# Kernel optimization log

Measured on AMD Instinct MI355X. Metric: run time of the kernel, lower is better.

Reference implementation:

```python
import jax, jax.numpy as jnp
import numpy as np

S, B, D, H, WIN, L = 8192, 4, 512, 8, 64, 6
HD = D // H
EPS = 1e-5


def setup_inputs() -> dict:
    key = jax.random.key(0)
    ks = jax.random.split(key, 6)
    s = 0.02
    return {
        "src": jax.random.normal(ks[0], (S, B, D), jnp.float32),
        "Wqkv": jax.random.normal(ks[1], (L, 3 * D, D), jnp.float32) * s,
        "bqkv": jnp.zeros((L, 3 * D), jnp.float32),
        "Wo": jax.random.normal(ks[2], (L, D, D), jnp.float32) * s,
        "bo": jnp.zeros((L, D), jnp.float32),
        "W1": jax.random.normal(ks[3], (L, 4 * D, D), jnp.float32) * s,
        "bf1": jnp.zeros((L, 4 * D), jnp.float32),
        "W2": jax.random.normal(ks[4], (L, D, 4 * D), jnp.float32) * s,
        "bf2": jnp.zeros((L, D), jnp.float32),
        "g1": jnp.ones((L, D), jnp.float32),
        "beta1": jnp.zeros((L, D), jnp.float32),
        "g2": jnp.ones((L, D), jnp.float32),
        "beta2": jnp.zeros((L, D), jnp.float32),
    }


def layernorm(x, g, b):
    m = jnp.mean(x, axis=-1, keepdims=True)
    v = jnp.mean(jnp.square(x - m), axis=-1, keepdims=True)
    return (x - m) * jax.lax.rsqrt(v + EPS) * g + b


def _forward(src, Wqkv, bqkv, Wo, bo, W1, bf1, W2, bf2, g1, beta1, g2, beta2):
    NW = S // WIN
    scale = 1.0 / np.sqrt(HD)
    x = src
    for l in range(L):
        qkv = x @ Wqkv[l].T + bqkv[l]                      # (S,B,3D)
        q, k, v = jnp.split(qkv, 3, axis=-1)
        win = lambda t: t.reshape(NW, WIN, B, H, HD)       # (NW,W,B,H,hd)
        q = win(q) * scale
        k = win(k)
        v = win(v)
        att = jax.nn.softmax(jnp.einsum('nqbhd,nkbhd->nbhqk', q, k), axis=-1)
        o = jnp.einsum('nbhqk,nkbhd->nqbhd', att, v).reshape(S, B, D)
        o = o @ Wo[l].T + bo[l]
        x = layernorm(x + o, g1[l], beta1[l])
        # FFN with ReLU (hidden = 4*d_model)
        f = jax.nn.relu(x @ W1[l].T + bf1[l]) @ W2[l].T + bf2[l]
        x = layernorm(x + f, g2[l], beta2[l])
    return x


def reference(src, Wqkv, bqkv, Wo, bo, W1, bf1, W2, bf2, g1, beta1, g2, beta2):
    return _forward(src, Wqkv, bqkv, Wo, bo, W1, bf1, W2, bf2, g1, beta1, g2, beta2)
```

## Files before the change

### kernel.cpp

```cpp
#include <hip/hip_runtime.h>
#include <hip/hip_bf16.h>

typedef __bf16 bf16x8 __attribute__((ext_vector_type(8)));
typedef float f32x4 __attribute__((ext_vector_type(4)));

static constexpr int NT = 32768;
static constexpr int D_ = 512;
static constexpr int D3 = 1536;
static constexpr int DF = 2048;
static constexpr int L_ = 6;

#define AS1 __attribute__((address_space(1)))
#define AS3 __attribute__((address_space(3)))

__device__ __forceinline__ void gload_lds16(const void* g, void* l) {
  __builtin_amdgcn_global_load_lds((const AS1 void*)g, (AS3 void*)l, 16, 0, 0);
}

template<int K, int NTILES, bool RELU>
__global__ __launch_bounds__(256, 2) void gemm_bt(
    const __hip_bfloat16* __restrict__ A,
    const __hip_bfloat16* __restrict__ W,
    const float* __restrict__ bias,
    __hip_bfloat16* __restrict__ Cout) {
  __shared__ __align__(16) __hip_bfloat16 lds[2 * 128 * 64];
  __hip_bfloat16* ldsA = lds;
  __hip_bfloat16* ldsB = lds + 128 * 64;
  const int t = threadIdx.x;
  const int l = t & 63, w = t >> 6;
  const int lrow = l & 15, lhi = l >> 4;

  const int lin = blockIdx.x;
  const int wg = (lin & 7) * ((int)gridDim.x >> 3) + (lin >> 3);
  const int tm0 = (wg / NTILES) * 128, tn0 = (wg % NTILES) * 128;
  const int wr = (w >> 1) * 64, wc = (w & 1) * 64;

  f32x4 acc[4][4] = {};

  const int nkt = K / 64;
  for (int kt = 0; kt < nkt; ++kt) {
    const int kbase = kt * 64;
    if (kt) __syncthreads();
#pragma unroll
    for (int i = 0; i < 4; ++i) {
      int slot = i * 256 + t;
      int row = slot >> 3, unit = slot & 7;
      int gc = kbase + ((unit ^ (row & 7)) << 3);
      gload_lds16(A + (size_t)(tm0 + row) * K + gc,
                  (char*)ldsA + i * 4096 + w * 1024);
    }
#pragma unroll
    for (int i = 0; i < 4; ++i) {
      int slot = i * 256 + t;
      int row = slot >> 3, unit = slot & 7;
      int gc = kbase + ((unit ^ (row & 7)) << 3);
      gload_lds16(W + (size_t)(tn0 + row) * K + gc,
                  (char*)ldsB + i * 4096 + w * 1024);
    }
    __syncthreads();

    bf16x8 af[4][2], bfr[4][2];
#pragma unroll
    for (int mi = 0; mi < 4; ++mi) {
      int r = wr + mi * 16 + lrow;
#pragma unroll
      for (int ks = 0; ks < 2; ++ks) {
        int unit = ks * 4 + lhi;
        af[mi][ks] = *(const bf16x8*)((const char*)ldsA + r * 128 + ((unit ^ (r & 7)) << 4));
      }
    }
#pragma unroll
    for (int ni = 0; ni < 4; ++ni) {
      int r = wc + ni * 16 + lrow;
#pragma unroll
      for (int ks = 0; ks < 2; ++ks) {
        int unit = ks * 4 + lhi;
        bfr[ni][ks] = *(const bf16x8*)((const char*)ldsB + r * 128 + ((unit ^ (r & 7)) << 4));
      }
    }
#pragma unroll
    for (int mi = 0; mi < 4; ++mi)
#pragma unroll
      for (int ni = 0; ni < 4; ++ni) {
        acc[mi][ni] = __builtin_amdgcn_mfma_f32_16x16x32_bf16(af[mi][0], bfr[ni][0], acc[mi][ni], 0, 0, 0);
        acc[mi][ni] = __builtin_amdgcn_mfma_f32_16x16x32_bf16(af[mi][1], bfr[ni][1], acc[mi][ni], 0, 0, 0);
      }
  }

  __syncthreads();
  char* ep = (char*)lds + w * 8192;
#pragma unroll
  for (int ni = 0; ni < 4; ++ni) {
    float bv = bias[tn0 + wc + ni * 16 + lrow];
#pragma unroll
    for (int mi = 0; mi < 4; ++mi) {
#pragma unroll
      for (int j = 0; j < 4; ++j) {
        float v = acc[mi][ni][j] + bv;
        if (RELU) v = fmaxf(v, 0.f);
        *(__hip_bfloat16*)(ep + (mi * 16 + lhi * 4 + j) * 128 + (ni * 16 + lrow) * 2) =
            __float2bfloat16(v);
      }
    }
  }
  const int er = l >> 3, ec = l & 7;
#pragma unroll
  for (int p = 0; p < 8; ++p) {
    int r = p * 8 + er;
    uint4 vv = *(const uint4*)(ep + r * 128 + ec * 16);
    *(uint4*)&Cout[(size_t)(tm0 + wr + r) * (NTILES * 128) + tn0 + wc + ec * 8] = vv;
  }
}

__global__ __launch_bounds__(128) void attn_win(
    const __hip_bfloat16* __restrict__ qkv, __hip_bfloat16* __restrict__ o) {
  __shared__ __align__(16) char lds[2 * 18432];
  const int t = threadIdx.x, l = t & 63, w = t >> 6;
  char* vt = lds + w * 18432;
  char* pl = vt + 9216;
  const int wid = blockIdx.x * 2 + w;
  const int h = wid & 7, b = (wid >> 3) & 3, nw = wid >> 5;
  const int lrow = l & 15, lhi = l >> 4;
  const __hip_bfloat16* qp = qkv + (size_t)(nw * 256 + b) * 1536 + h * 64;
  const __hip_bfloat16* kp = qp + 512;
  const __hip_bfloat16* vp = qp + 1024;

  {
    const int d0 = (l & 7) * 8;
    const int r0 = l >> 3;
#pragma unroll
    for (int i = 0; i < 8; ++i) {
      int r = r0 + i * 8;
      union { uint4 u; __hip_bfloat16 e[8]; } vv;
      vv.u = *(const uint4*)(vp + (size_t)r * 6144 + d0);
#pragma unroll
      for (int j = 0; j < 8; ++j)
        *(__hip_bfloat16*)(vt + ((d0 + j) * 72 + r) * 2) = vv.e[j];
    }
  }

  bf16x8 qf[4][2], kf[4][2];
#pragma unroll
  for (int mi = 0; mi < 4; ++mi)
#pragma unroll
    for (int ks = 0; ks < 2; ++ks) {
      int r = mi * 16 + lrow;
      int d = ks * 32 + lhi * 8;
      qf[mi][ks] = __builtin_bit_cast(bf16x8, *(const uint4*)(qp + (size_t)r * 6144 + d));
      kf[mi][ks] = __builtin_bit_cast(bf16x8, *(const uint4*)(kp + (size_t)r * 6144 + d));
    }

  f32x4 s[4][4] = {};
#pragma unroll
  for (int mi = 0; mi < 4; ++mi)
#pragma unroll
    for (int ni = 0; ni < 4; ++ni) {
      s[mi][ni] = __builtin_amdgcn_mfma_f32_16x16x32_bf16(qf[mi][0], kf[ni][0], s[mi][ni], 0, 0, 0);
      s[mi][ni] = __builtin_amdgcn_mfma_f32_16x16x32_bf16(qf[mi][1], kf[ni][1], s[mi][ni], 0, 0, 0);
    }

#pragma unroll
  for (int mi = 0; mi < 4; ++mi)
#pragma unroll
    for (int j = 0; j < 4; ++j) {
      float mx = s[mi][0][j];
#pragma unroll
      for (int ni = 1; ni < 4; ++ni) mx = fmaxf(mx, s[mi][ni][j]);
      mx = fmaxf(mx, __shfl_xor(mx, 1));
      mx = fmaxf(mx, __shfl_xor(mx, 2));
      mx = fmaxf(mx, __shfl_xor(mx, 4));
      mx = fmaxf(mx, __shfl_xor(mx, 8));
      float p[4], sum = 0.f;
#pragma unroll
      for (int ni = 0; ni < 4; ++ni) { p[ni] = __expf(s[mi][ni][j] - mx); sum += p[ni]; }
      sum += __shfl_xor(sum, 1);
      sum += __shfl_xor(sum, 2);
      sum += __shfl_xor(sum, 4);
      sum += __shfl_xor(sum, 8);
      float inv = 1.f / sum;
      int row = mi * 16 + lhi * 4 + j;
#pragma unroll
      for (int ni = 0; ni < 4; ++ni)
        *(__hip_bfloat16*)(pl + (row * 72 + ni * 16 + lrow) * 2) =
            __float2bfloat16(p[ni] * inv);
    }

  bf16x8 pf[4][2], vf[4][2];
#pragma unroll
  for (int mi = 0; mi < 4; ++mi)
#pragma unroll
    for (int ks = 0; ks < 2; ++ks)
      pf[mi][ks] = *(const bf16x8*)(pl + ((mi * 16 + lrow) * 72 + ks * 32 + lhi * 8) * 2);
#pragma unroll
  for (int ni = 0; ni < 4; ++ni)
#pragma unroll
    for (int ks = 0; ks < 2; ++ks)
      vf[ni][ks] = *(const bf16x8*)(vt + ((ni * 16 + lrow) * 72 + ks * 32 + lhi * 8) * 2);

  f32x4 acc[4][4] = {};
#pragma unroll
  for (int mi = 0; mi < 4; ++mi)
#pragma unroll
    for (int ni = 0; ni < 4; ++ni) {
      acc[mi][ni] = __builtin_amdgcn_mfma_f32_16x16x32_bf16(pf[mi][0], vf[ni][0], acc[mi][ni], 0, 0, 0);
      acc[mi][ni] = __builtin_amdgcn_mfma_f32_16x16x32_bf16(pf[mi][1], vf[ni][1], acc[mi][ni], 0, 0, 0);
    }

  __hip_bfloat16* op = o + (size_t)(nw * 256 + b) * 512 + h * 64;
#pragma unroll
  for (int mi = 0; mi < 4; ++mi)
#pragma unroll
    for (int ni = 0; ni < 4; ++ni) {
      int col = ni * 16 + lrow;
#pragma unroll
      for (int j = 0; j < 4; ++j) {
        int row = mi * 16 + lhi * 4 + j;
        op[(size_t)row * 2048 + col] = __float2bfloat16(acc[mi][ni][j]);
      }
    }
}

__global__ __launch_bounds__(256) void ln_res(
    float* __restrict__ x, const __hip_bfloat16* __restrict__ f,
    const float* __restrict__ g, const float* __restrict__ be,
    __hip_bfloat16* __restrict__ xb) {
  const int w = threadIdx.x >> 6, l = threadIdx.x & 63;
  const size_t row = (size_t)blockIdx.x * 4 + w;
  float* xr = x + row * 512;
  const int c = l * 8;
  float4 a0 = *(const float4*)(xr + c);
  float4 a1 = *(const float4*)(xr + c + 4);
  union { uint4 u; __hip_bfloat16 e[8]; } fb;
  fb.u = *(const uint4*)(f + row * 512 + c);
  float v[8] = {a0.x + __bfloat162float(fb.e[0]), a0.y + __bfloat162float(fb.e[1]),
                a0.z + __bfloat162float(fb.e[2]), a0.w + __bfloat162float(fb.e[3]),
                a1.x + __bfloat162float(fb.e[4]), a1.y + __bfloat162float(fb.e[5]),
                a1.z + __bfloat162float(fb.e[6]), a1.w + __bfloat162float(fb.e[7])};
  float sum = 0.f, sq = 0.f;
#pragma unroll
  for (int j = 0; j < 8; ++j) { sum += v[j]; sq += v[j] * v[j]; }
#pragma unroll
  for (int m = 1; m < 64; m <<= 1) {
    sum += __shfl_xor(sum, m);
    sq += __shfl_xor(sq, m);
  }
  float mean = sum * (1.f / 512.f);
  float var = sq * (1.f / 512.f) - mean * mean;
  float rs = rsqrtf(var + 1e-5f);
  float4 g0 = *(const float4*)(g + c);
  float4 g1v = *(const float4*)(g + c + 4);
  float4 e0 = *(const float4*)(be + c);
  float4 e1 = *(const float4*)(be + c + 4);
  float gg[8] = {g0.x, g0.y, g0.z, g0.w, g1v.x, g1v.y, g1v.z, g1v.w};
  float ee[8] = {e0.x, e0.y, e0.z, e0.w, e1.x, e1.y, e1.z, e1.w};
  float y[8];
  __hip_bfloat16 hb[8];
#pragma unroll
  for (int j = 0; j < 8; ++j) {
    y[j] = (v[j] - mean) * rs * gg[j] + ee[j];
    hb[j] = __float2bfloat16(y[j]);
  }
  float4 o0 = {y[0], y[1], y[2], y[3]};
  float4 o1 = {y[4], y[5], y[6], y[7]};
  *(float4*)(xr + c) = o0;
  *(float4*)(xr + c + 4) = o1;
  *(uint4*)((char*)(xb + row * 512 + c)) = *(uint4*)hb;
}

__global__ void bfc(const float* __restrict__ xm, __hip_bfloat16* __restrict__ xb) {
  int i = blockIdx.x * 256 + threadIdx.x;
  float4 v = ((const float4*)xm)[i];
  __hip_bfloat16 hb[4] = {__float2bfloat16(v.x), __float2bfloat16(v.y),
                          __float2bfloat16(v.z), __float2bfloat16(v.w)};
  ((uint2*)xb)[i] = *(uint2*)hb;
}

__global__ void convq(const float* __restrict__ wq, __hip_bfloat16* __restrict__ o) {
  int i = blockIdx.x * 256 + threadIdx.x;
  float4 v = ((const float4*)wq)[i];
  int e = i * 4;
  float sc = (((e >> 9) % 1536) < 512) ? 0.125f : 1.f;
  __hip_bfloat16 hb[4] = {__float2bfloat16(v.x * sc), __float2bfloat16(v.y * sc),
                          __float2bfloat16(v.z * sc), __float2bfloat16(v.w * sc)};
  ((uint2*)o)[i] = *(uint2*)hb;
}

__global__ void convw(const float* __restrict__ s, __hip_bfloat16* __restrict__ o) {
  int i = blockIdx.x * 256 + threadIdx.x;
  float4 v = ((const float4*)s)[i];
  __hip_bfloat16 hb[4] = {__float2bfloat16(v.x), __float2bfloat16(v.y),
                          __float2bfloat16(v.z), __float2bfloat16(v.w)};
  ((uint2*)o)[i] = *(uint2*)hb;
}

__global__ void scaleb(const float* __restrict__ b, float* __restrict__ o) {
  int i = blockIdx.x * 256 + threadIdx.x;
  o[i] = b[i] * (((i % 1536) < 512) ? 0.125f : 1.f);
}

extern "C" void kernel_launch(void* const* d_in, const int* in_sizes, int n_in,
                              void* d_out, int out_size, void* d_ws, size_t ws_size,
                              hipStream_t stream) {
  const float* src  = (const float*)d_in[0];
  const float* Wqkv = (const float*)d_in[1];
  const float* bqkv = (const float*)d_in[2];
  const float* Wo   = (const float*)d_in[3];
  const float* bo   = (const float*)d_in[4];
  const float* W1   = (const float*)d_in[5];
  const float* bf1  = (const float*)d_in[6];
  const float* W2   = (const float*)d_in[7];
  const float* bf2  = (const float*)d_in[8];
  const float* g1   = (const float*)d_in[9];
  const float* be1  = (const float*)d_in[10];
  const float* g2   = (const float*)d_in[11];
  const float* be2  = (const float*)d_in[12];
  float* x = (float*)d_out;

  char* ws = (char*)d_ws;
  size_t off = 0;
  auto alloc = [&](size_t bytes) {
    char* p = ws + off;
    off += (bytes + 255) & ~(size_t)255;
    return p;
  };

  const size_t wq_b = (size_t)L_ * D3 * D_ * 2;
  const size_t wo_b = (size_t)L_ * D_ * D_ * 2;
  const size_t w1_b = (size_t)L_ * DF * D_ * 2;
  const size_t w2_b = (size_t)L_ * D_ * DF * 2;
  auto al = [](size_t v) { return (v + 255) & ~(size_t)255; };
  const size_t persist = al(wq_b) + al(wo_b) + al(w1_b) + al(w2_b) + al(L_ * D3 * 4);

  int CT = NT;
  while (CT > 2048 && persist + (size_t)CT * 6144 + 65536 > ws_size) CT >>= 1;

  __hip_bfloat16* wqkvb = (__hip_bfloat16*)alloc(wq_b);
  __hip_bfloat16* wob   = (__hip_bfloat16*)alloc(wo_b);
  __hip_bfloat16* w1b   = (__hip_bfloat16*)alloc(w1_b);
  __hip_bfloat16* w2b   = (__hip_bfloat16*)alloc(w2_b);
  float*          bqs   = (float*)alloc((size_t)L_ * D3 * 4);
  __hip_bfloat16* xbf   = (__hip_bfloat16*)alloc((size_t)CT * 512 * 2);
  __hip_bfloat16* R     = (__hip_bfloat16*)alloc((size_t)CT * 2048 * 2);
  __hip_bfloat16* OB    = (__hip_bfloat16*)alloc((size_t)CT * 512 * 2);

  hipMemcpyAsync(x, src, (size_t)NT * 512 * 4, hipMemcpyDeviceToDevice, stream);
  convq<<<L_ * D3 * D_ / 4 / 256, 256, 0, stream>>>(Wqkv, wqkvb);
  convw<<<L_ * D_ * D_ / 4 / 256, 256, 0, stream>>>(Wo, wob);
  convw<<<L_ * DF * D_ / 4 / 256, 256, 0, stream>>>(W1, w1b);
  convw<<<L_ * D_ * DF / 4 / 256, 256, 0, stream>>>(W2, w2b);
  scaleb<<<L_ * D3 / 256, 256, 0, stream>>>(bqkv, bqs);

  const int nch = NT / CT;
  for (int c = 0; c < nch; ++c) {
    float* xm = x + (size_t)c * CT * 512;
    bfc<<<CT / 2, 256, 0, stream>>>(xm, xbf);
    for (int l = 0; l < L_; ++l) {
      gemm_bt<512, 12, false><<<(CT / 128) * 12, 256, 0, stream>>>(
          xbf, wqkvb + (size_t)l * D3 * D_, bqs + l * D3, R);
      attn_win<<<CT / 16, 128, 0, stream>>>(R, OB);
      gemm_bt<512, 4, false><<<(CT / 128) * 4, 256, 0, stream>>>(
          OB, wob + (size_t)l * D_ * D_, bo + l * D_, R);
      ln_res<<<CT / 4, 256, 0, stream>>>(xm, R, g1 + l * D_, be1 + l * D_, xbf);
      gemm_bt<512, 16, true><<<(CT / 128) * 16, 256, 0, stream>>>(
          xbf, w1b + (size_t)l * DF * D_, bf1 + l * DF, R);
      gemm_bt<2048, 4, false><<<(CT / 128) * 4, 256, 0, stream>>>(
          R, w2b + (size_t)l * D_ * DF, bf2 + l * D_, OB);
      ln_res<<<CT / 4, 256, 0, stream>>>(xm, OB, g2 + l * D_, be2 + l * D_, xbf);
    }
  }
}
```

Measured before the change: 2.143 ms.

## Replace 128x128 GEMM with double-buffered 256x256 tile, 8-wave pipelined kernel

Replaces the single-buffered 128x128 GEMM with a 256x256-tile, 512-thread kernel that double-buffers K tiles in 128KB of LDS. Global-to-LDS loads for later tiles are interleaved with the MFMA phases using explicit waitcnt, barriers and setprio. The larger tile raises data reuse per load, and the overlap hides load latency behind compute. The output epilogue also gains an XOR swizzle to avoid LDS bank conflicts. The cost is heavy LDS use, which limits occupancy to about one block per CU, and fewer blocks in the grid for the narrow GEMMs.

Result: faster. 2.024 ms (-5.6%).

```diff
diff --git a/kernel.cpp b/kernel.cpp
--- a/kernel.cpp
+++ b/kernel.cpp
@@ -17,98 +17,137 @@
   __builtin_amdgcn_global_load_lds((const AS1 void*)g, (AS3 void*)l, 16, 0, 0);
 }
 
-template<int K, int NTILES, bool RELU>
-__global__ __launch_bounds__(256, 2) void gemm_bt(
+template<int K, int NTN, bool RELU>
+__global__ __launch_bounds__(512, 2) void gemm256(
     const __hip_bfloat16* __restrict__ A,
     const __hip_bfloat16* __restrict__ W,
     const float* __restrict__ bias,
     __hip_bfloat16* __restrict__ Cout) {
-  __shared__ __align__(16) __hip_bfloat16 lds[2 * 128 * 64];
-  __hip_bfloat16* ldsA = lds;
-  __hip_bfloat16* ldsB = lds + 128 * 64;
+  __shared__ __align__(16) char lds[131072];
   const int t = threadIdx.x;
   const int l = t & 63, w = t >> 6;
   const int lrow = l & 15, lhi = l >> 4;
+  const int wr = w >> 2, wc = w & 3;
 
   const int lin = blockIdx.x;
   const int wg = (lin & 7) * ((int)gridDim.x >> 3) + (lin >> 3);
-  const int tm0 = (wg / NTILES) * 128, tn0 = (wg % NTILES) * 128;
-  const int wr = (w >> 1) * 64, wc = (w & 1) * 64;
-
-  f32x4 acc[4][4] = {};
-
-  const int nkt = K / 64;
-  for (int kt = 0; kt < nkt; ++kt) {
-    const int kbase = kt * 64;
-    if (kt) __syncthreads();
-#pragma unroll
-    for (int i = 0; i < 4; ++i) {
-      int slot = i * 256 + t;
-      int row = slot >> 3, unit = slot & 7;
-      int gc = kbase + ((unit ^ (row & 7)) << 3);
-      gload_lds16(A + (size_t)(tm0 + row) * K + gc,
-                  (char*)ldsA + i * 4096 + w * 1024);
-    }
-#pragma unroll
-    for (int i = 0; i < 4; ++i) {
-      int slot = i * 256 + t;
-      int row = slot >> 3, unit = slot & 7;
-      int gc = kbase + ((unit ^ (row & 7)) << 3);
-      gload_lds16(W + (size_t)(tn0 + row) * K + gc,
-                  (char*)ldsB + i * 4096 + w * 1024);
-    }
-    __syncthreads();
-
-    bf16x8 af[4][2], bfr[4][2];
-#pragma unroll
-    for (int mi = 0; mi < 4; ++mi) {
-      int r = wr + mi * 16 + lrow;
-#pragma unroll
-      for (int ks = 0; ks < 2; ++ks) {
-        int unit = ks * 4 + lhi;
-        af[mi][ks] = *(const bf16x8*)((const char*)ldsA + r * 128 + ((unit ^ (r & 7)) << 4));
+  const int tm0 = (wg / NTN) * 256, tn0 = (wg % NTN) * 256;
+
+  constexpr int NKT = K / 64;
+  constexpr int NIT = NKT / 2;
+  constexpr int N = NTN * 256;
+
+  const int srow = t >> 3;
+  const int sun = t & 7;
+
+  auto stage = [&](int buf, int reg, const __hip_bfloat16* P, int grow0, int tile) {
+    const int kb = tile * 64;
+    char* dst = lds + (buf * 4 + reg) * 16384 + w * 1024;
+#pragma unroll
+    for (int pass = 0; pass < 2; ++pass) {
+      int rl = pass * 64 + srow;
+      int u = sun ^ (rl & 7);
+      gload_lds16(P + (size_t)(grow0 + rl) * K + kb + u * 8, dst + pass * 8192);
+    }
+  };
+  auto rdA = [&](int buf, int m, int ks) -> bf16x8 {
+    int r = m * 16 + lrow;
+    return *(const bf16x8*)(lds + (buf * 4 + wr) * 16384 + r * 128 +
+                            (((ks * 4 + lhi) ^ (r & 7)) << 4));
+  };
+  auto rdB = [&](int buf, int n, int ks) -> bf16x8 {
+    int r = (wc & 1) * 64 + n * 16 + lrow;
+    return *(const bf16x8*)(lds + (buf * 4 + 2 + (wc >> 1)) * 16384 + r * 128 +
+                            (((ks * 4 + lhi) ^ (r & 7)) << 4));
+  };
+
+  f32x4 acc[8][4] = {};
+  bf16x8 bfrag[4][2], afrag[2][2];
+
+  stage(0, 2, W, tn0, 0);
+  stage(0, 3, W, tn0 + 128, 0);
+  stage(0, 0, A, tm0, 0);
+  stage(0, 1, A, tm0 + 128, 0);
+  stage(1, 2, W, tn0, 1);
+  stage(1, 3, W, tn0 + 128, 1);
+  asm volatile("s_waitcnt vmcnt(4)" ::: "memory");
+  __builtin_amdgcn_s_barrier();
+
+#define GPHASE(BUF, MB, RB, STG, VMS)                                       \
+  {                                                                          \
+    if (RB) {                                                                \
+      _Pragma("unroll") for (int n = 0; n < 4; ++n)                          \
+          _Pragma("unroll") for (int ks = 0; ks < 2; ++ks)                   \
+              bfrag[n][ks] = rdB(BUF, n, ks);                                \
+    }                                                                        \
+    _Pragma("unroll") for (int ks = 0; ks < 2; ++ks) {                       \
+      afrag[0][ks] = rdA(BUF, MB, ks);                                       \
+      afrag[1][ks] = rdA(BUF, MB + 1, ks);                                   \
+    }                                                                        \
+    STG;                                                                     \
+    VMS;                                                                     \
+    __builtin_amdgcn_sched_barrier(0);                                       \
+    __builtin_amdgcn_s_barrier();                                            \
+    asm volatile("s_waitcnt lgkmcnt(0)" ::: "memory");                       \
+    __builtin_amdgcn_sched_barrier(0);                                       \
+    __builtin_amdgcn_s_setprio(1);                                           \
+    _Pragma("unroll") for (int n = 0; n < 4; ++n)                            \
+        _Pragma("unroll") for (int ks = 0; ks < 2; ++ks) {                   \
+      acc[MB][n] = __builtin_amdgcn_mfma_f32_16x16x32_bf16(                  \
+          afrag[0][ks], bfrag[n][ks], acc[MB][n], 0, 0, 0);                  \
+      acc[MB + 1][n] = __builtin_amdgcn_mfma_f32_16x16x32_bf16(              \
+          afrag[1][ks], bfrag[n][ks], acc[MB + 1][n], 0, 0, 0);              \
+    }                                                                        \
+    __builtin_amdgcn_s_setprio(0);                                           \
+    __builtin_amdgcn_sched_barrier(0);                                       \
+    __builtin_amdgcn_s_barrier();                                            \
+  }
+
+#define VM_CNT                                              \
+  if (more) {                                               \
+    asm volatile("s_waitcnt vmcnt(4)" ::: "memory");        \
+  } else {                                                  \
+    asm volatile("s_waitcnt vmcnt(0)" ::: "memory");        \
+  }
+
+  for (int it = 0; it < NIT; ++it) {
+    const int t0 = 2 * it, t1 = 2 * it + 1;
+    const bool more = (it + 1 < NIT);
+    GPHASE(0, 0, 1, { stage(1, 0, A, tm0, t1); stage(1, 1, A, tm0 + 128, t1); }, );
+    GPHASE(0, 2, 0, { if (more) stage(0, 2, W, tn0, t0 + 2); }, );
+    GPHASE(0, 4, 0, { if (more) stage(0, 3, W, tn0 + 128, t0 + 2); }, );
+    GPHASE(0, 6, 0, , VM_CNT);
+    GPHASE(1, 0, 1, { if (more) stage(0, 0, A, tm0, t0 + 2); }, );
+    GPHASE(1, 2, 0, { if (more) stage(0, 1, A, tm0 + 128, t0 + 2); }, );
+    GPHASE(1, 4, 0, { if (more) stage(1, 2, W, tn0, t1 + 2); }, );
+    GPHASE(1, 6, 0, { if (more) stage(1, 3, W, tn0 + 128, t1 + 2); }, VM_CNT);
+  }
+#undef GPHASE
+#undef VM_CNT
+
+  char* ep = lds + w * 16384;
+#pragma unroll
+  for (int n = 0; n < 4; ++n) {
+    float bv = bias[tn0 + wc * 64 + n * 16 + lrow];
+#pragma unroll
+    for (int m = 0; m < 8; ++m)
+#pragma unroll
+      for (int j = 0; j < 4; ++j) {
+        float v = acc[m][n][j] + bv;
+        if (RELU) v = fmaxf(v, 0.f);
+        int row = m * 16 + lhi * 4 + j;
+        int col = n * 16 + lrow;
+        *(__hip_bfloat16*)(ep + row * 128 + (((col >> 3) ^ (row & 7)) << 4) +
+                           (col & 7) * 2) = __float2bfloat16(v);
       }
-    }
-#pragma unroll
-    for (int ni = 0; ni < 4; ++ni) {
-      int r = wc + ni * 16 + lrow;
-#pragma unroll
-      for (int ks = 0; ks < 2; ++ks) {
-        int unit = ks * 4 + lhi;
-        bfr[ni][ks] = *(const bf16x8*)((const char*)ldsB + r * 128 + ((unit ^ (r & 7)) << 4));
-      }
-    }
-#pragma unroll
-    for (int mi = 0; mi < 4; ++mi)
-#pragma unroll
-      for (int ni = 0; ni < 4; ++ni) {
-        acc[mi][ni] = __builtin_amdgcn_mfma_f32_16x16x32_bf16(af[mi][0], bfr[ni][0], acc[mi][ni], 0, 0, 0);
-        acc[mi][ni] = __builtin_amdgcn_mfma_f32_16x16x32_bf16(af[mi][1], bfr[ni][1], acc[mi][ni], 0, 0, 0);
-      }
-  }
-
-  __syncthreads();
-  char* ep = (char*)lds + w * 8192;
-#pragma unroll
-  for (int ni = 0; ni < 4; ++ni) {
-    float bv = bias[tn0 + wc + ni * 16 + lrow];
-#pragma unroll
-    for (int mi = 0; mi < 4; ++mi) {
-#pragma unroll
-      for (int j = 0; j < 4; ++j) {
-        float v = acc[mi][ni][j] + bv;
-        if (RELU) v = fmaxf(v, 0.f);
-        *(__hip_bfloat16*)(ep + (mi * 16 + lhi * 4 + j) * 128 + (ni * 16 + lrow) * 2) =
-            __float2bfloat16(v);
-      }
-    }
-  }
+  }
+  __builtin_amdgcn_sched_barrier(0);
   const int er = l >> 3, ec = l & 7;
 #pragma unroll
-  for (int p = 0; p < 8; ++p) {
+  for (int p = 0; p < 16; ++p) {
     int r = p * 8 + er;
-    uint4 vv = *(const uint4*)(ep + r * 128 + ec * 16);
-    *(uint4*)&Cout[(size_t)(tm0 + wr + r) * (NTILES * 128) + tn0 + wc + ec * 8] = vv;
+    uint4 vv = *(const uint4*)(ep + r * 128 + ((ec ^ (r & 7)) << 4));
+    *(uint4*)&Cout[(size_t)(tm0 + wr * 128 + r) * N + tn0 + wc * 64 + ec * 8] = vv;
   }
 }
 
@@ -355,15 +394,15 @@
     float* xm = x + (size_t)c * CT * 512;
     bfc<<<CT / 2, 256, 0, stream>>>(xm, xbf);
     for (int l = 0; l < L_; ++l) {
-      gemm_bt<512, 12, false><<<(CT / 128) * 12, 256, 0, stream>>>(
+      gemm256<512, 6, false><<<(CT / 256) * 6, 512, 0, stream>>>(
           xbf, wqkvb + (size_t)l * D3 * D_, bqs + l * D3, R);
       attn_win<<<CT / 16, 128, 0, stream>>>(R, OB);
-      gemm_bt<512, 4, false><<<(CT / 128) * 4, 256, 0, stream>>>(
+      gemm256<512, 2, false><<<(CT / 256) * 2, 512, 0, stream>>>(
           OB, wob + (size_t)l * D_ * D_, bo + l * D_, R);
       ln_res<<<CT / 4, 256, 0, stream>>>(xm, R, g1 + l * D_, be1 + l * D_, xbf);
-      gemm_bt<512, 16, true><<<(CT / 128) * 16, 256, 0, stream>>>(
+      gemm256<512, 8, true><<<(CT / 256) * 8, 512, 0, stream>>>(
           xbf, w1b + (size_t)l * DF * D_, bf1 + l * DF, R);
-      gemm_bt<2048, 4, false><<<(CT / 128) * 4, 256, 0, stream>>>(
+      gemm256<2048, 2, false><<<(CT / 256) * 2, 512, 0, stream>>>(
           R, w2b + (size_t)l * D_ * DF, bf2 + l * D_, OB);
       ln_res<<<CT / 4, 256, 0, stream>>>(xm, OB, g2 + l * D_, be2 + l * D_, xbf);
     }
```
